# Performance work log

Measured on AMD Instinct MI355X. Metric: run time of the kernel, lower is better.

Reference implementation:

```python
import jax, jax.numpy as jnp
import numpy as np

N_NODES = 50000
N_EDGES = 640000
D_IN = 128
D_OUT = 128


def setup_inputs() -> dict:
    key = jax.random.key(0)
    k1, k2, k3, k4, k5, k6 = jax.random.split(key, 6)
    nfeat = jax.random.normal(k1, (N_NODES, D_IN), dtype=jnp.float32)
    w = jax.random.uniform(k2, (N_EDGES,), dtype=jnp.float32)
    # nn.Linear weights are [out_feats, in_feats], Kaiming-uniform-ish scale
    bound = 1.0 / np.sqrt(D_IN)
    W1 = jax.random.uniform(k3, (D_OUT, D_IN), dtype=jnp.float32, minval=-bound, maxval=bound)
    W2 = jax.random.uniform(k4, (D_OUT, D_IN), dtype=jnp.float32, minval=-bound, maxval=bound)
    src = jax.random.randint(k5, (N_EDGES,), 0, N_NODES, dtype=jnp.int64)
    dst = jax.random.randint(k6, (N_EDGES,), 0, N_NODES, dtype=jnp.int64)
    return {"nfeat": nfeat, "w": w, "W1": W1, "W2": W2, "src": src, "dst": dst}


def reference(nfeat, w, W1, W2, src, dst):
    # feat_drop is identity in eval mode
    h = nfeat  # [N, D_IN]
    # update_all(u_mul_e('h','w','m'), sum('m','h_neighbor')):
    # gather source features, scale by per-edge scalar weight, scatter-sum to dst
    msg = h[src] * w[:, None]                                   # [E, D_IN]
    h_neighbor = jax.ops.segment_sum(msg, dst, num_segments=h.shape[0])  # [N, D_IN]
    # Bi-interaction residual: leaky_relu(Linear(h + hn)) + leaky_relu(Linear(h * hn))
    add_branch = jax.nn.leaky_relu((h + h_neighbor) @ W1.T, negative_slope=0.01)
    mul_branch = jax.nn.leaky_relu((h * h_neighbor) @ W2.T, negative_slope=0.01)
    out = add_branch + mul_branch                                # [N, D_OUT]
    return (h_neighbor, out)
```

## Files before the change

kernel.cpp:

```cpp
#include <hip/hip_runtime.h>
#include <hip/hip_bf16.h>

#define N_NODES 50000
#define N_EDGES 640000
#define D 128
#define OUT0_ELEMS (N_NODES * D)
#define SCAN_BLOCKS ((N_NODES + 255) / 256)

typedef __attribute__((ext_vector_type(8))) short short8v;
typedef __attribute__((ext_vector_type(4))) short short4v;
typedef __attribute__((ext_vector_type(4))) float f32x4;

static __device__ __forceinline__ unsigned short f2bf(float x) {
  __hip_bfloat16 b = __float2bfloat16(x);
  return *reinterpret_cast<unsigned short*>(&b);
}
static __device__ __forceinline__ float bf2f(unsigned short u) {
  unsigned x = ((unsigned)u) << 16;
  return __builtin_bit_cast(float, x);
}
static __device__ __forceinline__ unsigned pack_edge(int s, float wv) {
  return ((unsigned)f2bf(wv) << 16) | (unsigned)s;
}

__global__ __launch_bounds__(256) void conv_all(
    const float* __restrict__ nfeat, const float* __restrict__ W1,
    const float* __restrict__ W2, unsigned short* __restrict__ nf16,
    unsigned short* __restrict__ wc, int* __restrict__ cnt) {
  int i = blockIdx.x * 256 + threadIdx.x;
  int base = i * 8;
  float4 a = *(const float4*)(nfeat + base);
  float4 b = *(const float4*)(nfeat + base + 4);
  short8v o;
  o[0] = (short)f2bf(a.x); o[1] = (short)f2bf(a.y);
  o[2] = (short)f2bf(a.z); o[3] = (short)f2bf(a.w);
  o[4] = (short)f2bf(b.x); o[5] = (short)f2bf(b.y);
  o[6] = (short)f2bf(b.z); o[7] = (short)f2bf(b.w);
  *(short8v*)(nf16 + base) = o;
  if (i < D * D) {
    wc[i] = f2bf(W1[i]);
    wc[D * D + i] = f2bf(W2[i]);
  }
  if (i < N_NODES) cnt[i] = 0;
}

__global__ __launch_bounds__(256) void hist_rank(
    const int* __restrict__ dst, int* __restrict__ cnt, int* __restrict__ rank) {
  int t = blockIdx.x * 256 + threadIdx.x;
  int e = t * 4;
  if (e >= N_EDGES) return;
  int4 d4 = *(const int4*)(dst + e);
  int4 r4;
  r4.x = atomicAdd(&cnt[d4.x], 1);
  r4.y = atomicAdd(&cnt[d4.y], 1);
  r4.z = atomicAdd(&cnt[d4.z], 1);
  r4.w = atomicAdd(&cnt[d4.w], 1);
  *(int4*)(rank + e) = r4;
}

__global__ __launch_bounds__(256) void scan_block(
    const int* __restrict__ cnt, int* __restrict__ offs, int* __restrict__ bsums) {
  __shared__ int sdata[256];
  int t = threadIdx.x;
  int i = blockIdx.x * 256 + t;
  int v = (i < N_NODES) ? cnt[i] : 0;
  sdata[t] = v;
  __syncthreads();
#pragma unroll
  for (int off = 1; off < 256; off <<= 1) {
    int x = (t >= off) ? sdata[t - off] : 0;
    __syncthreads();
    sdata[t] += x;
    __syncthreads();
  }
  if (i < N_NODES) offs[i] = sdata[t] - v;
  if (t == 255) bsums[blockIdx.x] = sdata[t];
}

__global__ __launch_bounds__(256) void scan_top(int* __restrict__ bsums) {
  __shared__ int sdata[256];
  int t = threadIdx.x;
  int v = (t < SCAN_BLOCKS) ? bsums[t] : 0;
  sdata[t] = v;
  __syncthreads();
#pragma unroll
  for (int off = 1; off < 256; off <<= 1) {
    int x = (t >= off) ? sdata[t - off] : 0;
    __syncthreads();
    sdata[t] += x;
    __syncthreads();
  }
  if (t < SCAN_BLOCKS) bsums[t] = sdata[t] - v;
}

__global__ __launch_bounds__(256) void scan_finalize(
    int* __restrict__ offs, const int* __restrict__ bsums) {
  int i = blockIdx.x * 256 + threadIdx.x;
  if (i >= N_NODES) return;
  offs[i] += bsums[blockIdx.x];
  if (i == N_NODES - 1) offs[N_NODES] = N_EDGES;
}

__global__ __launch_bounds__(256) void fill4(
    const int* __restrict__ src, const int* __restrict__ dst,
    const float* __restrict__ w, const int* __restrict__ rank,
    const int* __restrict__ offs, unsigned* __restrict__ es) {
  int t = blockIdx.x * 256 + threadIdx.x;
  int e = t * 4;
  if (e >= N_EDGES) return;
  int4 d4 = *(const int4*)(dst + e);
  int4 r4 = *(const int4*)(rank + e);
  int4 s4 = *(const int4*)(src + e);
  float4 w4 = *(const float4*)(w + e);
  es[offs[d4.x] + r4.x] = pack_edge(s4.x, w4.x);
  es[offs[d4.y] + r4.y] = pack_edge(s4.y, w4.y);
  es[offs[d4.z] + r4.z] = pack_edge(s4.z, w4.z);
  es[offs[d4.w] + r4.w] = pack_edge(s4.w, w4.w);
}

__global__ __launch_bounds__(256) void gather_bf16(
    const unsigned short* __restrict__ nf16, const int* __restrict__ offs,
    const unsigned* __restrict__ es, float* __restrict__ hn) {
  int tid = blockIdx.x * 256 + threadIdx.x;
  int node = tid >> 4;
  if (node >= N_NODES) return;
  int q = tid & 15;
  int beg = offs[node];
  int end = offs[node + 1];
  float acc[8];
#pragma unroll
  for (int j = 0; j < 8; ++j) acc[j] = 0.f;

  int k = beg;
  for (; k + 3 < end; k += 4) {
    unsigned r0 = es[k], r1 = es[k + 1], r2 = es[k + 2], r3 = es[k + 3];
    short8v v0 = *(const short8v*)(nf16 + (size_t)(r0 & 0xFFFF) * D + q * 8);
    short8v v1 = *(const short8v*)(nf16 + (size_t)(r1 & 0xFFFF) * D + q * 8);
    short8v v2 = *(const short8v*)(nf16 + (size_t)(r2 & 0xFFFF) * D + q * 8);
    short8v v3 = *(const short8v*)(nf16 + (size_t)(r3 & 0xFFFF) * D + q * 8);
    float w0 = bf2f((unsigned short)(r0 >> 16));
    float w1 = bf2f((unsigned short)(r1 >> 16));
    float w2 = bf2f((unsigned short)(r2 >> 16));
    float w3 = bf2f((unsigned short)(r3 >> 16));
#pragma unroll
    for (int j = 0; j < 8; ++j) {
      acc[j] += bf2f((unsigned short)v0[j]) * w0;
      acc[j] += bf2f((unsigned short)v1[j]) * w1;
      acc[j] += bf2f((unsigned short)v2[j]) * w2;
      acc[j] += bf2f((unsigned short)v3[j]) * w3;
    }
  }
  for (; k < end; ++k) {
    unsigned r0 = es[k];
    short8v v0 = *(const short8v*)(nf16 + (size_t)(r0 & 0xFFFF) * D + q * 8);
    float w0 = bf2f((unsigned short)(r0 >> 16));
#pragma unroll
    for (int j = 0; j < 8; ++j) acc[j] += bf2f((unsigned short)v0[j]) * w0;
  }

  float* orow = hn + (size_t)node * D + q * 8;
  *(float4*)(orow) = make_float4(acc[0], acc[1], acc[2], acc[3]);
  *(float4*)(orow + 4) = make_float4(acc[4], acc[5], acc[6], acc[7]);
}

__global__ __launch_bounds__(256) void gather_f32(
    const float* __restrict__ nfeat, const int* __restrict__ offs,
    const unsigned* __restrict__ es, float* __restrict__ hn) {
  int tid = blockIdx.x * 256 + threadIdx.x;
  int node = tid >> 5;
  if (node >= N_NODES) return;
  int q = tid & 31;
  int beg = offs[node];
  int end = offs[node + 1];
  float4 acc = {0.f, 0.f, 0.f, 0.f};
  int k = beg;
  for (; k + 1 < end; k += 2) {
    unsigned r0 = es[k], r1 = es[k + 1];
    float w0 = bf2f((unsigned short)(r0 >> 16));
    float w1 = bf2f((unsigned short)(r1 >> 16));
    float4 v0 = ((const float4*)(nfeat + (size_t)(r0 & 0xFFFF) * D))[q];
    float4 v1 = ((const float4*)(nfeat + (size_t)(r1 & 0xFFFF) * D))[q];
    acc.x += v0.x * w0 + v1.x * w1;
    acc.y += v0.y * w0 + v1.y * w1;
    acc.z += v0.z * w0 + v1.z * w1;
    acc.w += v0.w * w0 + v1.w * w1;
  }
  if (k < end) {
    unsigned r0 = es[k];
    float w0 = bf2f((unsigned short)(r0 >> 16));
    float4 v0 = ((const float4*)(nfeat + (size_t)(r0 & 0xFFFF) * D))[q];
    acc.x += v0.x * w0;
    acc.y += v0.y * w0;
    acc.z += v0.z * w0;
    acc.w += v0.w * w0;
  }
  ((float4*)(hn + (size_t)node * D))[q] = acc;
}

__global__ __launch_bounds__(256) void wconv(
    const float* __restrict__ W1, const float* __restrict__ W2,
    unsigned short* __restrict__ wc, int* __restrict__ cnt) {
  int i = blockIdx.x * 256 + threadIdx.x;
  if (i < D * D) {
    wc[i] = f2bf(W1[i]);
    wc[D * D + i] = f2bf(W2[i]);
  }
  if (i < N_NODES) cnt[i] = 0;
}

template <bool HBF16>
__global__ __launch_bounds__(256) void bi_mfma(
    const void* __restrict__ hsrc, const float* __restrict__ hn,
    const unsigned short* __restrict__ wc, float* __restrict__ out) {
  __shared__ __align__(16) unsigned short lds[2 * 64 * D];

  const int tid = threadIdx.x;
  const int lane = tid & 63;
  const int wid = tid >> 6;
  const int base = blockIdx.x * 64;
  const int r16 = lane & 15;
  const int kg = lane >> 4;

  short8v bf[2][2][4];
  {
    const int colbase = wid * 32;
#pragma unroll
    for (int g = 0; g < 2; ++g)
#pragma unroll
      for (int c = 0; c < 2; ++c)
#pragma unroll
        for (int ks = 0; ks < 4; ++ks) {
          int col = colbase + c * 16 + r16;
          int k = ks * 32 + kg * 8;
          bf[g][c][ks] =
              *(const short8v*)(wc + (size_t)g * D * D + (size_t)col * D + k);
        }
  }

#pragma unroll
  for (int p = 0; p < 8; ++p) {
    int flat = p * 1024 + tid * 4;
    int row = flat >> 7;
    int col = flat & 127;
    int node = base + row;
    float hx0 = 0.f, hx1 = 0.f, hx2 = 0.f, hx3 = 0.f;
    float4 nv = make_float4(0.f, 0.f, 0.f, 0.f);
    if (node < N_NODES) {
      if constexpr (HBF16) {
        short4v hv =
            *(const short4v*)((const unsigned short*)hsrc + (size_t)node * D + col);
        hx0 = bf2f((unsigned short)hv[0]);
        hx1 = bf2f((unsigned short)hv[1]);
        hx2 = bf2f((unsigned short)hv[2]);
        hx3 = bf2f((unsigned short)hv[3]);
      } else {
        float4 hv = *(const float4*)((const float*)hsrc + (size_t)node * D + col);
        hx0 = hv.x; hx1 = hv.y; hx2 = hv.z; hx3 = hv.w;
      }
      nv = *(const float4*)(hn + (size_t)node * D + col);
    }
    short4v av, mv;
    av[0] = (short)f2bf(hx0 + nv.x);
    av[1] = (short)f2bf(hx1 + nv.y);
    av[2] = (short)f2bf(hx2 + nv.z);
    av[3] = (short)f2bf(hx3 + nv.w);
    mv[0] = (short)f2bf(hx0 * nv.x);
    mv[1] = (short)f2bf(hx1 * nv.y);
    mv[2] = (short)f2bf(hx2 * nv.z);
    mv[3] = (short)f2bf(hx3 * nv.w);
    int boff = (row * 256 + col * 2) ^ ((row & 7) << 4);
    *(short4v*)((char*)lds + boff) = av;
    *(short4v*)((char*)lds + 16384 + boff) = mv;
  }
  __syncthreads();

  f32x4 acc1[4][2], acc2[4][2];
#pragma unroll
  for (int rt = 0; rt < 4; ++rt)
#pragma unroll
    for (int c = 0; c < 2; ++c) {
      acc1[rt][c] = (f32x4){0.f, 0.f, 0.f, 0.f};
      acc2[rt][c] = (f32x4){0.f, 0.f, 0.f, 0.f};
    }

#pragma unroll
  for (int ks = 0; ks < 4; ++ks) {
#pragma unroll
    for (int rt = 0; rt < 4; ++rt) {
      int row = rt * 16 + r16;
      int boff = (row * 256 + (ks * 32 + kg * 8) * 2) ^ ((row & 7) << 4);
      short8v a1 = *(const short8v*)((const char*)lds + boff);
      short8v a2 = *(const short8v*)((const char*)lds + 16384 + boff);
#pragma unroll
      for (int c = 0; c < 2; ++c) {
        acc1[rt][c] = __builtin_amdgcn_mfma_f32_16x16x32_bf16(
            a1, bf[0][c][ks], acc1[rt][c], 0, 0, 0);
        acc2[rt][c] = __builtin_amdgcn_mfma_f32_16x16x32_bf16(
            a2, bf[1][c][ks], acc2[rt][c], 0, 0, 0);
      }
    }
  }

#pragma unroll
  for (int rt = 0; rt < 4; ++rt) {
#pragma unroll
    for (int c = 0; c < 2; ++c) {
#pragma unroll
      for (int e = 0; e < 4; ++e) {
        int row = rt * 16 + kg * 4 + e;
        int node = base + row;
        if (node < N_NODES) {
          int col = wid * 32 + c * 16 + r16;
          float x1 = acc1[rt][c][e];
          float x2 = acc2[rt][c][e];
          x1 = x1 > 0.f ? x1 : 0.01f * x1;
          x2 = x2 > 0.f ? x2 : 0.01f * x2;
          out[(size_t)node * D + col] = x1 + x2;
        }
      }
    }
  }
}

__global__ __launch_bounds__(256) void edge_scatter(
    const float* __restrict__ nfeat, const float* __restrict__ w,
    const int* __restrict__ src, const int* __restrict__ dst,
    float* __restrict__ hn) {
  int tid = blockIdx.x * 256 + threadIdx.x;
  int e = tid >> 5;
  if (e >= N_EDGES) return;
  int q = tid & 31;
  int s = src[e];
  int d = dst[e];
  float we = w[e];
  float4 v = ((const float4*)(nfeat + (size_t)s * D))[q];
  float* drow = hn + (size_t)d * D + q * 4;
  atomicAdd(drow + 0, v.x * we);
  atomicAdd(drow + 1, v.y * we);
  atomicAdd(drow + 2, v.z * we);
  atomicAdd(drow + 3, v.w * we);
}

__global__ __launch_bounds__(256) void bi_inter(
    const float* __restrict__ h, const float* __restrict__ hn,
    const float* __restrict__ W1, const float* __restrict__ W2,
    float* __restrict__ out) {
  int wid = __builtin_amdgcn_readfirstlane(threadIdx.x >> 6);
  int lane = threadIdx.x & 63;
  int node = blockIdx.x * 64 + lane;
  if (node >= N_NODES) return;
  const float4* h4 = (const float4*)(h + (size_t)node * D);
  const float4* n4 = (const float4*)(hn + (size_t)node * D);
  float acc1[32], acc2[32];
#pragma unroll
  for (int j = 0; j < 32; ++j) { acc1[j] = 0.f; acc2[j] = 0.f; }
  const int obase = wid * 32;
  for (int kq = 0; kq < 32; ++kq) {
    float4 hv = h4[kq];
    float4 nv = n4[kq];
    float a0 = hv.x + nv.x, a1 = hv.y + nv.y, a2 = hv.z + nv.z, a3 = hv.w + nv.w;
    float m0 = hv.x * nv.x, m1 = hv.y * nv.y, m2 = hv.z * nv.z, m3 = hv.w * nv.w;
#pragma unroll
    for (int j = 0; j < 32; ++j) {
      int o = obase + j;
      float4 w1 = *(const float4*)(W1 + (size_t)o * D + kq * 4);
      float4 w2 = *(const float4*)(W2 + (size_t)o * D + kq * 4);
      acc1[j] += a0 * w1.x + a1 * w1.y + a2 * w1.z + a3 * w1.w;
      acc2[j] += m0 * w2.x + m1 * w2.y + m2 * w2.z + m3 * w2.w;
    }
  }
  float* orow = out + (size_t)node * D + obase;
#pragma unroll
  for (int j = 0; j < 32; j += 4) {
    float4 r;
    float x;
    x = acc1[j + 0]; x = x > 0.f ? x : 0.01f * x;
    r.x = x; x = acc2[j + 0]; x = x > 0.f ? x : 0.01f * x; r.x += x;
    x = acc1[j + 1]; x = x > 0.f ? x : 0.01f * x;
    r.y = x; x = acc2[j + 1]; x = x > 0.f ? x : 0.01f * x; r.y += x;
    x = acc1[j + 2]; x = x > 0.f ? x : 0.01f * x;
    r.z = x; x = acc2[j + 2]; x = x > 0.f ? x : 0.01f * x; r.z += x;
    x = acc1[j + 3]; x = x > 0.f ? x : 0.01f * x;
    r.w = x; x = acc2[j + 3]; x = x > 0.f ? x : 0.01f * x; r.w += x;
    *(float4*)(orow + j) = r;
  }
}

extern "C" void kernel_launch(void* const* d_in, const int* in_sizes, int n_in,
                              void* d_out, int out_size, void* d_ws, size_t ws_size,
                              hipStream_t stream) {
  const float* nfeat = (const float*)d_in[0];
  const float* w     = (const float*)d_in[1];
  const float* W1    = (const float*)d_in[2];
  const float* W2    = (const float*)d_in[3];
  const int*   src   = (const int*)d_in[4];
  const int*   dst   = (const int*)d_in[5];

  float* hn  = (float*)d_out;
  float* out = (float*)d_out + OUT0_ELEMS;

  char* ws = (char*)d_ws;
  size_t off = 0;
  int* cnt = (int*)(ws + off);        off += (size_t)N_NODES * 4;
  int* offs = (int*)(ws + off);       off += (size_t)(N_NODES + 1) * 4;
  int* bsums = (int*)(ws + off);      off += 256 * 4;
  int* rank = (int*)(ws + off);       off += (size_t)N_EDGES * 4;
  unsigned* es = (unsigned*)(ws + off); off += (size_t)N_EDGES * 4;
  off = (off + 63) & ~(size_t)63;
  unsigned short* wc = (unsigned short*)(ws + off);
  off += (size_t)2 * D * D * 2;
  size_t tier1_bytes = off;
  off = (off + 63) & ~(size_t)63;
  unsigned short* nf16 = (unsigned short*)(ws + off);
  off += (size_t)N_NODES * D * 2;
  size_t tier2_bytes = off;

  if (ws_size < tier1_bytes) {
    hipMemsetAsync(hn, 0, (size_t)OUT0_ELEMS * sizeof(float), stream);
    long long threads = (long long)N_EDGES * 32;
    int blocks = (int)((threads + 255) / 256);
    edge_scatter<<<blocks, 256, 0, stream>>>(nfeat, w, src, dst, hn);
    bi_inter<<<(N_NODES + 63) / 64, 256, 0, stream>>>(nfeat, hn, W1, W2, out);
    return;
  }

  bool full = (ws_size >= tier2_bytes);

  if (full) {
    conv_all<<<N_NODES * D / 8 / 256, 256, 0, stream>>>(
        nfeat, W1, W2, nf16, wc, cnt);
  } else {
    wconv<<<(N_NODES + 255) / 256, 256, 0, stream>>>(W1, W2, wc, cnt);
  }
  hist_rank<<<N_EDGES / 4 / 256, 256, 0, stream>>>(dst, cnt, rank);
  scan_block<<<SCAN_BLOCKS, 256, 0, stream>>>(cnt, offs, bsums);
  scan_top<<<1, 256, 0, stream>>>(bsums);
  scan_finalize<<<SCAN_BLOCKS, 256, 0, stream>>>(offs, bsums);
  fill4<<<N_EDGES / 4 / 256, 256, 0, stream>>>(src, dst, w, rank, offs, es);

  if (full) {
    gather_bf16<<<(N_NODES * 16 + 255) / 256, 256, 0, stream>>>(nf16, offs, es, hn);
    bi_mfma<true><<<(N_NODES + 63) / 64, 256, 0, stream>>>(nf16, hn, wc, out);
  } else {
    gather_f32<<<(N_NODES * 32 + 255) / 256, 256, 0, stream>>>(nfeat, offs, es, hn);
    bi_mfma<false><<<(N_NODES + 63) / 64, 256, 0, stream>>>(nfeat, hn, wc, out);
  }
}
```

Baseline: 111.1 us.

## Fuse neighbor gather into bi-interaction MFMA kernel and collapse scan into one kernel

Merges the bf16 gather kernel with the bi-interaction MFMA kernel. Each block aggregates neighbor features for its 64 nodes, writes hn, and places h+hn and h*hn straight into LDS as bf16, so the MFMA stage no longer reads hn back from global memory. The three-kernel prefix scan is replaced by a single 256-thread block in which each thread serially scans a chunk of 196 counts. The cost is fewer, heavier gather blocks with lower parallelism (one node per 16 threads across 4 iterations), and a scan that runs serially on one block.

```diff
diff --git a/kernel.cpp b/kernel.cpp
--- a/kernel.cpp
+++ b/kernel.cpp
@@ -5,7 +5,7 @@
 #define N_EDGES 640000
 #define D 128
 #define OUT0_ELEMS (N_NODES * D)
-#define SCAN_BLOCKS ((N_NODES + 255) / 256)
+#define SCAN_CHUNK 196
 
 typedef __attribute__((ext_vector_type(8))) short short8v;
 typedef __attribute__((ext_vector_type(4))) short short4v;
@@ -58,13 +58,16 @@
   *(int4*)(rank + e) = r4;
 }
 
-__global__ __launch_bounds__(256) void scan_block(
-    const int* __restrict__ cnt, int* __restrict__ offs, int* __restrict__ bsums) {
+__global__ __launch_bounds__(256) void scan_one(
+    const int* __restrict__ cnt, int* __restrict__ offs) {
   __shared__ int sdata[256];
   int t = threadIdx.x;
-  int i = blockIdx.x * 256 + t;
-  int v = (i < N_NODES) ? cnt[i] : 0;
-  sdata[t] = v;
+  int beg = t * SCAN_CHUNK;
+  int end = beg + SCAN_CHUNK;
+  if (end > N_NODES) end = N_NODES;
+  int s = 0;
+  for (int i = beg; i < end; ++i) s += cnt[i];
+  sdata[t] = s;
   __syncthreads();
 #pragma unroll
   for (int off = 1; off < 256; off <<= 1) {
@@ -73,32 +76,12 @@
     sdata[t] += x;
     __syncthreads();
   }
-  if (i < N_NODES) offs[i] = sdata[t] - v;
-  if (t == 255) bsums[blockIdx.x] = sdata[t];
-}
-
-__global__ __launch_bounds__(256) void scan_top(int* __restrict__ bsums) {
-  __shared__ int sdata[256];
-  int t = threadIdx.x;
-  int v = (t < SCAN_BLOCKS) ? bsums[t] : 0;
-  sdata[t] = v;
-  __syncthreads();
-#pragma unroll
-  for (int off = 1; off < 256; off <<= 1) {
-    int x = (t >= off) ? sdata[t - off] : 0;
-    __syncthreads();
-    sdata[t] += x;
-    __syncthreads();
-  }
-  if (t < SCAN_BLOCKS) bsums[t] = sdata[t] - v;
-}
-
-__global__ __launch_bounds__(256) void scan_finalize(
-    int* __restrict__ offs, const int* __restrict__ bsums) {
-  int i = blockIdx.x * 256 + threadIdx.x;
-  if (i >= N_NODES) return;
-  offs[i] += bsums[blockIdx.x];
-  if (i == N_NODES - 1) offs[N_NODES] = N_EDGES;
+  int run = sdata[t] - s;
+  for (int i = beg; i < end; ++i) {
+    offs[i] = run;
+    run += cnt[i];
+  }
+  if (t == 0) offs[N_NODES] = N_EDGES;
 }
 
 __global__ __launch_bounds__(256) void fill4(
@@ -118,49 +101,156 @@
   es[offs[d4.w] + r4.w] = pack_edge(s4.w, w4.w);
 }
 
-__global__ __launch_bounds__(256) void gather_bf16(
+__global__ __launch_bounds__(256) void gather_bi(
     const unsigned short* __restrict__ nf16, const int* __restrict__ offs,
-    const unsigned* __restrict__ es, float* __restrict__ hn) {
-  int tid = blockIdx.x * 256 + threadIdx.x;
-  int node = tid >> 4;
-  if (node >= N_NODES) return;
-  int q = tid & 15;
-  int beg = offs[node];
-  int end = offs[node + 1];
-  float acc[8];
-#pragma unroll
-  for (int j = 0; j < 8; ++j) acc[j] = 0.f;
-
-  int k = beg;
-  for (; k + 3 < end; k += 4) {
-    unsigned r0 = es[k], r1 = es[k + 1], r2 = es[k + 2], r3 = es[k + 3];
-    short8v v0 = *(const short8v*)(nf16 + (size_t)(r0 & 0xFFFF) * D + q * 8);
-    short8v v1 = *(const short8v*)(nf16 + (size_t)(r1 & 0xFFFF) * D + q * 8);
-    short8v v2 = *(const short8v*)(nf16 + (size_t)(r2 & 0xFFFF) * D + q * 8);
-    short8v v3 = *(const short8v*)(nf16 + (size_t)(r3 & 0xFFFF) * D + q * 8);
-    float w0 = bf2f((unsigned short)(r0 >> 16));
-    float w1 = bf2f((unsigned short)(r1 >> 16));
-    float w2 = bf2f((unsigned short)(r2 >> 16));
-    float w3 = bf2f((unsigned short)(r3 >> 16));
+    const unsigned* __restrict__ es, const unsigned short* __restrict__ wc,
+    float* __restrict__ hn, float* __restrict__ out) {
+  __shared__ __align__(16) unsigned short lds[2 * 64 * D];
+
+  const int tid = threadIdx.x;
+  const int base = blockIdx.x * 64;
+  const int g = tid >> 4;
+  const int q = tid & 15;
+
+#pragma unroll
+  for (int i = 0; i < 4; ++i) {
+    int row = g * 4 + i;
+    int node = base + row;
+    float acc[8];
+#pragma unroll
+    for (int j = 0; j < 8; ++j) acc[j] = 0.f;
+    float hx[8];
+#pragma unroll
+    for (int j = 0; j < 8; ++j) hx[j] = 0.f;
+
+    if (node < N_NODES) {
+      int beg = offs[node];
+      int end = offs[node + 1];
+      int k = beg;
+      for (; k + 3 < end; k += 4) {
+        unsigned r0 = es[k], r1 = es[k + 1], r2 = es[k + 2], r3 = es[k + 3];
+        short8v v0 = *(const short8v*)(nf16 + (size_t)(r0 & 0xFFFF) * D + q * 8);
+        short8v v1 = *(const short8v*)(nf16 + (size_t)(r1 & 0xFFFF) * D + q * 8);
+        short8v v2 = *(const short8v*)(nf16 + (size_t)(r2 & 0xFFFF) * D + q * 8);
+        short8v v3 = *(const short8v*)(nf16 + (size_t)(r3 & 0xFFFF) * D + q * 8);
+        float w0 = bf2f((unsigned short)(r0 >> 16));
+        float w1 = bf2f((unsigned short)(r1 >> 16));
+        float w2 = bf2f((unsigned short)(r2 >> 16));
+        float w3 = bf2f((unsigned short)(r3 >> 16));
+#pragma unroll
+        for (int j = 0; j < 8; ++j) {
+          acc[j] += bf2f((unsigned short)v0[j]) * w0;
+          acc[j] += bf2f((unsigned short)v1[j]) * w1;
+          acc[j] += bf2f((unsigned short)v2[j]) * w2;
+          acc[j] += bf2f((unsigned short)v3[j]) * w3;
+        }
+      }
+      for (; k < end; ++k) {
+        unsigned r0 = es[k];
+        short8v v0 = *(const short8v*)(nf16 + (size_t)(r0 & 0xFFFF) * D + q * 8);
+        float w0 = bf2f((unsigned short)(r0 >> 16));
+#pragma unroll
+        for (int j = 0; j < 8; ++j) acc[j] += bf2f((unsigned short)v0[j]) * w0;
+      }
+
+      short8v hv = *(const short8v*)(nf16 + (size_t)node * D + q * 8);
+#pragma unroll
+      for (int j = 0; j < 8; ++j) hx[j] = bf2f((unsigned short)hv[j]);
+
+      float* orow = hn + (size_t)node * D + q * 8;
+      *(float4*)(orow) = make_float4(acc[0], acc[1], acc[2], acc[3]);
+      *(float4*)(orow + 4) = make_float4(acc[4], acc[5], acc[6], acc[7]);
+    }
+
+    short8v av, mv;
 #pragma unroll
     for (int j = 0; j < 8; ++j) {
-      acc[j] += bf2f((unsigned short)v0[j]) * w0;
-      acc[j] += bf2f((unsigned short)v1[j]) * w1;
-      acc[j] += bf2f((unsigned short)v2[j]) * w2;
-      acc[j] += bf2f((unsigned short)v3[j]) * w3;
-    }
-  }
-  for (; k < end; ++k) {
-    unsigned r0 = es[k];
-    short8v v0 = *(const short8v*)(nf16 + (size_t)(r0 & 0xFFFF) * D + q * 8);
-    float w0 = bf2f((unsigned short)(r0 >> 16));
-#pragma unroll
-    for (int j = 0; j < 8; ++j) acc[j] += bf2f((unsigned short)v0[j]) * w0;
-  }
-
-  float* orow = hn + (size_t)node * D + q * 8;
-  *(float4*)(orow) = make_float4(acc[0], acc[1], acc[2], acc[3]);
-  *(float4*)(orow + 4) = make_float4(acc[4], acc[5], acc[6], acc[7]);
+      av[j] = (short)f2bf(hx[j] + acc[j]);
+      mv[j] = (short)f2bf(hx[j] * acc[j]);
+    }
+    int boff = (row * 256 + q * 16) ^ ((row & 7) << 4);
+    *(short8v*)((char*)lds + boff) = av;
+    *(short8v*)((char*)lds + 16384 + boff) = mv;
+  }
+
+  const int lane = tid & 63;
+  const int wid = tid >> 6;
+  const int r16 = lane & 15;
+  const int kg = lane >> 4;
+  short8v bf[2][2][4];
+  {
+    const int colbase = wid * 32;
+#pragma unroll
+    for (int gg = 0; gg < 2; ++gg)
+#pragma unroll
+      for (int c = 0; c < 2; ++c)
+#pragma unroll
+        for (int ks = 0; ks < 4; ++ks) {
+          int col = colbase + c * 16 + r16;
+          int k = ks * 32 + kg * 8;
+          bf[gg][c][ks] =
+              *(const short8v*)(wc + (size_t)gg * D * D + (size_t)col * D + k);
+        }
+  }
+  __syncthreads();
+
+  f32x4 acc1[4][2], acc2[4][2];
+#pragma unroll
+  for (int rt = 0; rt < 4; ++rt)
+#pragma unroll
+    for (int c = 0; c < 2; ++c) {
+      acc1[rt][c] = (f32x4){0.f, 0.f, 0.f, 0.f};
+      acc2[rt][c] = (f32x4){0.f, 0.f, 0.f, 0.f};
+    }
+
+#pragma unroll
+  for (int ks = 0; ks < 4; ++ks) {
+#pragma unroll
+    for (int rt = 0; rt < 4; ++rt) {
+      int row = rt * 16 + r16;
+      int boff = (row * 256 + (ks * 32 + kg * 8) * 2) ^ ((row & 7) << 4);
+      short8v a1 = *(const short8v*)((const char*)lds + boff);
+      short8v a2 = *(const short8v*)((const char*)lds + 16384 + boff);
+#pragma unroll
+      for (int c = 0; c < 2; ++c) {
+        acc1[rt][c] = __builtin_amdgcn_mfma_f32_16x16x32_bf16(
+            a1, bf[0][c][ks], acc1[rt][c], 0, 0, 0);
+        acc2[rt][c] = __builtin_amdgcn_mfma_f32_16x16x32_bf16(
+            a2, bf[1][c][ks], acc2[rt][c], 0, 0, 0);
+      }
+    }
+  }
+
+#pragma unroll
+  for (int rt = 0; rt < 4; ++rt) {
+#pragma unroll
+    for (int c = 0; c < 2; ++c) {
+#pragma unroll
+      for (int e = 0; e < 4; ++e) {
+        int row = rt * 16 + kg * 4 + e;
+        int node = base + row;
+        if (node < N_NODES) {
+          int col = wid * 32 + c * 16 + r16;
+          float x1 = acc1[rt][c][e];
+          float x2 = acc2[rt][c][e];
+          x1 = x1 > 0.f ? x1 : 0.01f * x1;
+          x2 = x2 > 0.f ? x2 : 0.01f * x2;
+          out[(size_t)node * D + col] = x1 + x2;
+        }
+      }
+    }
+  }
+}
+
+__global__ __launch_bounds__(256) void wconv(
+    const float* __restrict__ W1, const float* __restrict__ W2,
+    unsigned short* __restrict__ wc, int* __restrict__ cnt) {
+  int i = blockIdx.x * 256 + threadIdx.x;
+  if (i < D * D) {
+    wc[i] = f2bf(W1[i]);
+    wc[D * D + i] = f2bf(W2[i]);
+  }
+  if (i < N_NODES) cnt[i] = 0;
 }
 
 __global__ __launch_bounds__(256) void gather_f32(
@@ -197,46 +287,31 @@
   ((float4*)(hn + (size_t)node * D))[q] = acc;
 }
 
-__global__ __launch_bounds__(256) void wconv(
-    const float* __restrict__ W1, const float* __restrict__ W2,
-    unsigned short* __restrict__ wc, int* __restrict__ cnt) {
-  int i = blockIdx.x * 256 + threadIdx.x;
-  if (i < D * D) {
-    wc[i] = f2bf(W1[i]);
-    wc[D * D + i] = f2bf(W2[i]);
-  }
-  if (i < N_NODES) cnt[i] = 0;
-}
-
-template <bool HBF16>
-__global__ __launch_bounds__(256) void bi_mfma(
-    const void* __restrict__ hsrc, const float* __restrict__ hn,
+__global__ __launch_bounds__(256) void bi_mfma_f32(
+    const float* __restrict__ h, const float* __restrict__ hn,
     const unsigned short* __restrict__ wc, float* __restrict__ out) {
   __shared__ __align__(16) unsigned short lds[2 * 64 * D];
-
   const int tid = threadIdx.x;
   const int lane = tid & 63;
   const int wid = tid >> 6;
   const int base = blockIdx.x * 64;
   const int r16 = lane & 15;
   const int kg = lane >> 4;
-
   short8v bf[2][2][4];
   {
     const int colbase = wid * 32;
 #pragma unroll
-    for (int g = 0; g < 2; ++g)
+    for (int gg = 0; gg < 2; ++gg)
 #pragma unroll
       for (int c = 0; c < 2; ++c)
 #pragma unroll
         for (int ks = 0; ks < 4; ++ks) {
           int col = colbase + c * 16 + r16;
           int k = ks * 32 + kg * 8;
-          bf[g][c][ks] =
-              *(const short8v*)(wc + (size_t)g * D * D + (size_t)col * D + k);
+          bf[gg][c][ks] =
+              *(const short8v*)(wc + (size_t)gg * D * D + (size_t)col * D + k);
         }
   }
-
 #pragma unroll
   for (int p = 0; p < 8; ++p) {
     int flat = p * 1024 + tid * 4;
@@ -246,17 +321,8 @@
     float hx0 = 0.f, hx1 = 0.f, hx2 = 0.f, hx3 = 0.f;
     float4 nv = make_float4(0.f, 0.f, 0.f, 0.f);
     if (node < N_NODES) {
-      if constexpr (HBF16) {
-        short4v hv =
-            *(const short4v*)((const unsigned short*)hsrc + (size_t)node * D + col);
-        hx0 = bf2f((unsigned short)hv[0]);
-        hx1 = bf2f((unsigned short)hv[1]);
-        hx2 = bf2f((unsigned short)hv[2]);
-        hx3 = bf2f((unsigned short)hv[3]);
-      } else {
-        float4 hv = *(const float4*)((const float*)hsrc + (size_t)node * D + col);
-        hx0 = hv.x; hx1 = hv.y; hx2 = hv.z; hx3 = hv.w;
-      }
+      float4 hv = *(const float4*)(h + (size_t)node * D + col);
+      hx0 = hv.x; hx1 = hv.y; hx2 = hv.z; hx3 = hv.w;
       nv = *(const float4*)(hn + (size_t)node * D + col);
     }
     short4v av, mv;
@@ -273,7 +339,6 @@
     *(short4v*)((char*)lds + 16384 + boff) = mv;
   }
   __syncthreads();
-
   f32x4 acc1[4][2], acc2[4][2];
 #pragma unroll
   for (int rt = 0; rt < 4; ++rt)
@@ -282,7 +347,6 @@
       acc1[rt][c] = (f32x4){0.f, 0.f, 0.f, 0.f};
       acc2[rt][c] = (f32x4){0.f, 0.f, 0.f, 0.f};
     }
-
 #pragma unroll
   for (int ks = 0; ks < 4; ++ks) {
 #pragma unroll
@@ -300,7 +364,6 @@
       }
     }
   }
-
 #pragma unroll
   for (int rt = 0; rt < 4; ++rt) {
 #pragma unroll
@@ -401,10 +464,9 @@
 
   char* ws = (char*)d_ws;
   size_t off = 0;
-  int* cnt = (int*)(ws + off);        off += (size_t)N_NODES * 4;
-  int* offs = (int*)(ws + off);       off += (size_t)(N_NODES + 1) * 4;
-  int* bsums = (int*)(ws + off);      off += 256 * 4;
-  int* rank = (int*)(ws + off);       off += (size_t)N_EDGES * 4;
+  int* cnt = (int*)(ws + off);          off += (size_t)N_NODES * 4;
+  int* offs = (int*)(ws + off);         off += (size_t)(N_NODES + 1) * 4;
+  int* rank = (int*)(ws + off);         off += (size_t)N_EDGES * 4;
   unsigned* es = (unsigned*)(ws + off); off += (size_t)N_EDGES * 4;
   off = (off + 63) & ~(size_t)63;
   unsigned short* wc = (unsigned short*)(ws + off);
@@ -433,16 +495,13 @@
     wconv<<<(N_NODES + 255) / 256, 256, 0, stream>>>(W1, W2, wc, cnt);
   }
   hist_rank<<<N_EDGES / 4 / 256, 256, 0, stream>>>(dst, cnt, rank);
-  scan_block<<<SCAN_BLOCKS, 256, 0, stream>>>(cnt, offs, bsums);
-  scan_top<<<1, 256, 0, stream>>>(bsums);
-  scan_finalize<<<SCAN_BLOCKS, 256, 0, stream>>>(offs, bsums);
+  scan_one<<<1, 256, 0, stream>>>(cnt, offs);
   fill4<<<N_EDGES / 4 / 256, 256, 0, stream>>>(src, dst, w, rank, offs, es);
 
   if (full) {
-    gather_bf16<<<(N_NODES * 16 + 255) / 256, 256, 0, stream>>>(nf16, offs, es, hn);
-    bi_mfma<true><<<(N_NODES + 63) / 64, 256, 0, stream>>>(nf16, hn, wc, out);
+    gather_bi<<<(N_NODES + 63) / 64, 256, 0, stream>>>(nf16, offs, es, wc, hn, out);
   } else {
     gather_f32<<<(N_NODES * 32 + 255) / 256, 256, 0, stream>>>(nfeat, offs, es, hn);
-    bi_mfma<false><<<(N_NODES + 63) / 64, 256, 0, stream>>>(nfeat, hn, wc, out);
-  }
-}
+    bi_mfma_f32<<<(N_NODES + 63) / 64, 256, 0, stream>>>(nfeat, hn, wc, out);
+  }
+}
```

New measurement: 196.7 us. +77.1%, slower.

## Fuse CSR build stages into one persistent kernel with software grid barriers

Applied to the files above, without the earlier changes.

Merges the bf16 conversion, histogram/rank, two-level scan and edge fill kernels into a single persistent kernel of 512 blocks that separates phases with atomic-based grid barriers. The scan is restructured into per-block chunk sums, a single-block top scan, and a local rescan. The goal is to remove several kernel launches and the gaps between them. In exchange it relies on all 512 blocks being co-resident and adds barrier spin costs; the intermediate fp32 fallback tier is dropped.

```diff
diff --git a/kernel.cpp b/kernel.cpp
--- a/kernel.cpp
+++ b/kernel.cpp
@@ -5,7 +5,10 @@
 #define N_EDGES 640000
 #define D 128
 #define OUT0_ELEMS (N_NODES * D)
-#define SCAN_BLOCKS ((N_NODES + 255) / 256)
+
+#define CSR_BLOCKS 512
+#define CSR_THREADS (CSR_BLOCKS * 256)
+#define CHUNK 98
 
 typedef __attribute__((ext_vector_type(8))) short short8v;
 typedef __attribute__((ext_vector_type(4))) short short4v;
@@ -23,99 +26,128 @@
   return ((unsigned)f2bf(wv) << 16) | (unsigned)s;
 }
 
-__global__ __launch_bounds__(256) void conv_all(
+static __device__ __forceinline__ void grid_sync(int* bar, int phase) {
+  __syncthreads();
+  if (threadIdx.x == 0) {
+    int prev = __hip_atomic_fetch_add(&bar[0], 1, __ATOMIC_ACQ_REL,
+                                      __HIP_MEMORY_SCOPE_AGENT);
+    if (prev == (int)gridDim.x - 1) {
+      __hip_atomic_store(&bar[0], 0, __ATOMIC_RELAXED, __HIP_MEMORY_SCOPE_AGENT);
+      __hip_atomic_store(&bar[1], phase, __ATOMIC_RELEASE, __HIP_MEMORY_SCOPE_AGENT);
+    } else {
+      long long guard = 0;
+      while (__hip_atomic_load(&bar[1], __ATOMIC_ACQUIRE,
+                               __HIP_MEMORY_SCOPE_AGENT) < phase) {
+        __builtin_amdgcn_s_sleep(4);
+        if (++guard > (1LL << 28)) break;
+      }
+    }
+  }
+  __syncthreads();
+}
+
+__global__ __launch_bounds__(256, 2) void build_all(
     const float* __restrict__ nfeat, const float* __restrict__ W1,
-    const float* __restrict__ W2, unsigned short* __restrict__ nf16,
-    unsigned short* __restrict__ wc, int* __restrict__ cnt) {
-  int i = blockIdx.x * 256 + threadIdx.x;
-  int base = i * 8;
-  float4 a = *(const float4*)(nfeat + base);
-  float4 b = *(const float4*)(nfeat + base + 4);
-  short8v o;
-  o[0] = (short)f2bf(a.x); o[1] = (short)f2bf(a.y);
-  o[2] = (short)f2bf(a.z); o[3] = (short)f2bf(a.w);
-  o[4] = (short)f2bf(b.x); o[5] = (short)f2bf(b.y);
-  o[6] = (short)f2bf(b.z); o[7] = (short)f2bf(b.w);
-  *(short8v*)(nf16 + base) = o;
-  if (i < D * D) {
-    wc[i] = f2bf(W1[i]);
-    wc[D * D + i] = f2bf(W2[i]);
-  }
-  if (i < N_NODES) cnt[i] = 0;
-}
-
-__global__ __launch_bounds__(256) void hist_rank(
-    const int* __restrict__ dst, int* __restrict__ cnt, int* __restrict__ rank) {
-  int t = blockIdx.x * 256 + threadIdx.x;
-  int e = t * 4;
-  if (e >= N_EDGES) return;
-  int4 d4 = *(const int4*)(dst + e);
-  int4 r4;
-  r4.x = atomicAdd(&cnt[d4.x], 1);
-  r4.y = atomicAdd(&cnt[d4.y], 1);
-  r4.z = atomicAdd(&cnt[d4.z], 1);
-  r4.w = atomicAdd(&cnt[d4.w], 1);
-  *(int4*)(rank + e) = r4;
-}
-
-__global__ __launch_bounds__(256) void scan_block(
-    const int* __restrict__ cnt, int* __restrict__ offs, int* __restrict__ bsums) {
+    const float* __restrict__ W2, const int* __restrict__ src,
+    const int* __restrict__ dst, const float* __restrict__ w,
+    unsigned short* __restrict__ nf16, unsigned short* __restrict__ wc,
+    int* __restrict__ cnt, int* __restrict__ offs, int* __restrict__ rank,
+    unsigned* __restrict__ es, int* __restrict__ bsums, int* __restrict__ bar) {
+  const int tid = threadIdx.x;
+  const int t = blockIdx.x * 256 + tid;
   __shared__ int sdata[256];
-  int t = threadIdx.x;
-  int i = blockIdx.x * 256 + t;
-  int v = (i < N_NODES) ? cnt[i] : 0;
-  sdata[t] = v;
-  __syncthreads();
-#pragma unroll
-  for (int off = 1; off < 256; off <<= 1) {
-    int x = (t >= off) ? sdata[t - off] : 0;
+
+  if (t < N_NODES) cnt[t] = 0;
+  if (t < D * D) {
+    wc[t] = f2bf(W1[t]);
+    wc[D * D + t] = f2bf(W2[t]);
+  }
+  for (int u = t; u < N_NODES * D / 8; u += CSR_THREADS) {
+    int base = u * 8;
+    float4 a = *(const float4*)(nfeat + base);
+    float4 b = *(const float4*)(nfeat + base + 4);
+    short8v o;
+    o[0] = (short)f2bf(a.x); o[1] = (short)f2bf(a.y);
+    o[2] = (short)f2bf(a.z); o[3] = (short)f2bf(a.w);
+    o[4] = (short)f2bf(b.x); o[5] = (short)f2bf(b.y);
+    o[6] = (short)f2bf(b.z); o[7] = (short)f2bf(b.w);
+    *(short8v*)(nf16 + base) = o;
+  }
+  grid_sync(bar, 1);
+
+  for (int u = t; u < N_EDGES / 4; u += CSR_THREADS) {
+    int e = u * 4;
+    int4 d4 = *(const int4*)(dst + e);
+    int4 r4;
+    r4.x = atomicAdd(&cnt[d4.x], 1);
+    r4.y = atomicAdd(&cnt[d4.y], 1);
+    r4.z = atomicAdd(&cnt[d4.z], 1);
+    r4.w = atomicAdd(&cnt[d4.w], 1);
+    *(int4*)(rank + e) = r4;
+  }
+  grid_sync(bar, 2);
+
+  {
+    int i = blockIdx.x * CHUNK + tid;
+    int v = (tid < CHUNK && i < N_NODES) ? cnt[i] : 0;
+    sdata[tid] = v;
     __syncthreads();
-    sdata[t] += x;
+#pragma unroll
+    for (int o = 128; o > 0; o >>= 1) {
+      if (tid < o) sdata[tid] += sdata[tid + o];
+      __syncthreads();
+    }
+    if (tid == 0) bsums[blockIdx.x] = sdata[0];
+  }
+  grid_sync(bar, 3);
+
+  if (blockIdx.x == 0) {
+    int b0 = bsums[2 * tid], b1 = bsums[2 * tid + 1];
+    int p = b0 + b1;
+    sdata[tid] = p;
     __syncthreads();
-  }
-  if (i < N_NODES) offs[i] = sdata[t] - v;
-  if (t == 255) bsums[blockIdx.x] = sdata[t];
-}
-
-__global__ __launch_bounds__(256) void scan_top(int* __restrict__ bsums) {
-  __shared__ int sdata[256];
-  int t = threadIdx.x;
-  int v = (t < SCAN_BLOCKS) ? bsums[t] : 0;
-  sdata[t] = v;
-  __syncthreads();
-#pragma unroll
-  for (int off = 1; off < 256; off <<= 1) {
-    int x = (t >= off) ? sdata[t - off] : 0;
+#pragma unroll
+    for (int o = 1; o < 256; o <<= 1) {
+      int x = (tid >= o) ? sdata[tid - o] : 0;
+      __syncthreads();
+      sdata[tid] += x;
+      __syncthreads();
+    }
+    int excl = sdata[tid] - p;
+    bsums[2 * tid] = excl;
+    bsums[2 * tid + 1] = excl + b0;
+  }
+  grid_sync(bar, 4);
+
+  {
+    int i = blockIdx.x * CHUNK + tid;
+    int v = (tid < CHUNK && i < N_NODES) ? cnt[i] : 0;
+    sdata[tid] = v;
     __syncthreads();
-    sdata[t] += x;
-    __syncthreads();
-  }
-  if (t < SCAN_BLOCKS) bsums[t] = sdata[t] - v;
-}
-
-__global__ __launch_bounds__(256) void scan_finalize(
-    int* __restrict__ offs, const int* __restrict__ bsums) {
-  int i = blockIdx.x * 256 + threadIdx.x;
-  if (i >= N_NODES) return;
-  offs[i] += bsums[blockIdx.x];
-  if (i == N_NODES - 1) offs[N_NODES] = N_EDGES;
-}
-
-__global__ __launch_bounds__(256) void fill4(
-    const int* __restrict__ src, const int* __restrict__ dst,
-    const float* __restrict__ w, const int* __restrict__ rank,
-    const int* __restrict__ offs, unsigned* __restrict__ es) {
-  int t = blockIdx.x * 256 + threadIdx.x;
-  int e = t * 4;
-  if (e >= N_EDGES) return;
-  int4 d4 = *(const int4*)(dst + e);
-  int4 r4 = *(const int4*)(rank + e);
-  int4 s4 = *(const int4*)(src + e);
-  float4 w4 = *(const float4*)(w + e);
-  es[offs[d4.x] + r4.x] = pack_edge(s4.x, w4.x);
-  es[offs[d4.y] + r4.y] = pack_edge(s4.y, w4.y);
-  es[offs[d4.z] + r4.z] = pack_edge(s4.z, w4.z);
-  es[offs[d4.w] + r4.w] = pack_edge(s4.w, w4.w);
+#pragma unroll
+    for (int o = 1; o < 256; o <<= 1) {
+      int x = (tid >= o) ? sdata[tid - o] : 0;
+      __syncthreads();
+      sdata[tid] += x;
+      __syncthreads();
+    }
+    int excl = sdata[tid] - v + bsums[blockIdx.x];
+    if (tid < CHUNK && i < N_NODES) offs[i] = excl;
+    if (t == 0) offs[N_NODES] = N_EDGES;
+  }
+  grid_sync(bar, 5);
+
+  for (int u = t; u < N_EDGES / 4; u += CSR_THREADS) {
+    int e = u * 4;
+    int4 d4 = *(const int4*)(dst + e);
+    int4 r4 = *(const int4*)(rank + e);
+    int4 s4 = *(const int4*)(src + e);
+    float4 w4 = *(const float4*)(w + e);
+    es[offs[d4.x] + r4.x] = pack_edge(s4.x, w4.x);
+    es[offs[d4.y] + r4.y] = pack_edge(s4.y, w4.y);
+    es[offs[d4.z] + r4.z] = pack_edge(s4.z, w4.z);
+    es[offs[d4.w] + r4.w] = pack_edge(s4.w, w4.w);
+  }
 }
 
 __global__ __launch_bounds__(256) void gather_bf16(
@@ -163,54 +195,8 @@
   *(float4*)(orow + 4) = make_float4(acc[4], acc[5], acc[6], acc[7]);
 }
 
-__global__ __launch_bounds__(256) void gather_f32(
-    const float* __restrict__ nfeat, const int* __restrict__ offs,
-    const unsigned* __restrict__ es, float* __restrict__ hn) {
-  int tid = blockIdx.x * 256 + threadIdx.x;
-  int node = tid >> 5;
-  if (node >= N_NODES) return;
-  int q = tid & 31;
-  int beg = offs[node];
-  int end = offs[node + 1];
-  float4 acc = {0.f, 0.f, 0.f, 0.f};
-  int k = beg;
-  for (; k + 1 < end; k += 2) {
-    unsigned r0 = es[k], r1 = es[k + 1];
-    float w0 = bf2f((unsigned short)(r0 >> 16));
-    float w1 = bf2f((unsigned short)(r1 >> 16));
-    float4 v0 = ((const float4*)(nfeat + (size_t)(r0 & 0xFFFF) * D))[q];
-    float4 v1 = ((const float4*)(nfeat + (size_t)(r1 & 0xFFFF) * D))[q];
-    acc.x += v0.x * w0 + v1.x * w1;
-    acc.y += v0.y * w0 + v1.y * w1;
-    acc.z += v0.z * w0 + v1.z * w1;
-    acc.w += v0.w * w0 + v1.w * w1;
-  }
-  if (k < end) {
-    unsigned r0 = es[k];
-    float w0 = bf2f((unsigned short)(r0 >> 16));
-    float4 v0 = ((const float4*)(nfeat + (size_t)(r0 & 0xFFFF) * D))[q];
-    acc.x += v0.x * w0;
-    acc.y += v0.y * w0;
-    acc.z += v0.z * w0;
-    acc.w += v0.w * w0;
-  }
-  ((float4*)(hn + (size_t)node * D))[q] = acc;
-}
-
-__global__ __launch_bounds__(256) void wconv(
-    const float* __restrict__ W1, const float* __restrict__ W2,
-    unsigned short* __restrict__ wc, int* __restrict__ cnt) {
-  int i = blockIdx.x * 256 + threadIdx.x;
-  if (i < D * D) {
-    wc[i] = f2bf(W1[i]);
-    wc[D * D + i] = f2bf(W2[i]);
-  }
-  if (i < N_NODES) cnt[i] = 0;
-}
-
-template <bool HBF16>
-__global__ __launch_bounds__(256) void bi_mfma(
-    const void* __restrict__ hsrc, const float* __restrict__ hn,
+__global__ __launch_bounds__(256) void bi_mfma_h16(
+    const unsigned short* __restrict__ h16, const float* __restrict__ hn,
     const unsigned short* __restrict__ wc, float* __restrict__ out) {
   __shared__ __align__(16) unsigned short lds[2 * 64 * D];
 
@@ -246,17 +232,11 @@
     float hx0 = 0.f, hx1 = 0.f, hx2 = 0.f, hx3 = 0.f;
     float4 nv = make_float4(0.f, 0.f, 0.f, 0.f);
     if (node < N_NODES) {
-      if constexpr (HBF16) {
-        short4v hv =
-            *(const short4v*)((const unsigned short*)hsrc + (size_t)node * D + col);
-        hx0 = bf2f((unsigned short)hv[0]);
-        hx1 = bf2f((unsigned short)hv[1]);
-        hx2 = bf2f((unsigned short)hv[2]);
-        hx3 = bf2f((unsigned short)hv[3]);
-      } else {
-        float4 hv = *(const float4*)((const float*)hsrc + (size_t)node * D + col);
-        hx0 = hv.x; hx1 = hv.y; hx2 = hv.z; hx3 = hv.w;
-      }
+      short4v hv = *(const short4v*)(h16 + (size_t)node * D + col);
+      hx0 = bf2f((unsigned short)hv[0]);
+      hx1 = bf2f((unsigned short)hv[1]);
+      hx2 = bf2f((unsigned short)hv[2]);
+      hx3 = bf2f((unsigned short)hv[3]);
       nv = *(const float4*)(hn + (size_t)node * D + col);
     }
     short4v av, mv;
@@ -401,21 +381,21 @@
 
   char* ws = (char*)d_ws;
   size_t off = 0;
-  int* cnt = (int*)(ws + off);        off += (size_t)N_NODES * 4;
-  int* offs = (int*)(ws + off);       off += (size_t)(N_NODES + 1) * 4;
-  int* bsums = (int*)(ws + off);      off += 256 * 4;
-  int* rank = (int*)(ws + off);       off += (size_t)N_EDGES * 4;
+  int* bar = (int*)(ws + off);          off += 64;
+  int* bsums = (int*)(ws + off);        off += CSR_BLOCKS * 4;
+  int* cnt = (int*)(ws + off);          off += (size_t)N_NODES * 4;
+  int* offs = (int*)(ws + off);         off += (size_t)(N_NODES + 1) * 4;
+  int* rank = (int*)(ws + off);         off += (size_t)N_EDGES * 4;
   unsigned* es = (unsigned*)(ws + off); off += (size_t)N_EDGES * 4;
   off = (off + 63) & ~(size_t)63;
   unsigned short* wc = (unsigned short*)(ws + off);
   off += (size_t)2 * D * D * 2;
-  size_t tier1_bytes = off;
   off = (off + 63) & ~(size_t)63;
   unsigned short* nf16 = (unsigned short*)(ws + off);
   off += (size_t)N_NODES * D * 2;
-  size_t tier2_bytes = off;
-
-  if (ws_size < tier1_bytes) {
+  size_t full_bytes = off;
+
+  if (ws_size < full_bytes) {
     hipMemsetAsync(hn, 0, (size_t)OUT0_ELEMS * sizeof(float), stream);
     long long threads = (long long)N_EDGES * 32;
     int blocks = (int)((threads + 255) / 256);
@@ -424,25 +404,10 @@
     return;
   }
 
-  bool full = (ws_size >= tier2_bytes);
-
-  if (full) {
-    conv_all<<<N_NODES * D / 8 / 256, 256, 0, stream>>>(
-        nfeat, W1, W2, nf16, wc, cnt);
-  } else {
-    wconv<<<(N_NODES + 255) / 256, 256, 0, stream>>>(W1, W2, wc, cnt);
-  }
-  hist_rank<<<N_EDGES / 4 / 256, 256, 0, stream>>>(dst, cnt, rank);
-  scan_block<<<SCAN_BLOCKS, 256, 0, stream>>>(cnt, offs, bsums);
-  scan_top<<<1, 256, 0, stream>>>(bsums);
-  scan_finalize<<<SCAN_BLOCKS, 256, 0, stream>>>(offs, bsums);
-  fill4<<<N_EDGES / 4 / 256, 256, 0, stream>>>(src, dst, w, rank, offs, es);
-
-  if (full) {
-    gather_bf16<<<(N_NODES * 16 + 255) / 256, 256, 0, stream>>>(nf16, offs, es, hn);
-    bi_mfma<true><<<(N_NODES + 63) / 64, 256, 0, stream>>>(nf16, hn, wc, out);
-  } else {
-    gather_f32<<<(N_NODES * 32 + 255) / 256, 256, 0, stream>>>(nfeat, offs, es, hn);
-    bi_mfma<false><<<(N_NODES + 63) / 64, 256, 0, stream>>>(nfeat, hn, wc, out);
-  }
-}
+  hipMemsetAsync(bar, 0, 16, stream);
+
+  build_all<<<CSR_BLOCKS, 256, 0, stream>>>(
+      nfeat, W1, W2, src, dst, w, nf16, wc, cnt, offs, rank, es, bsums, bar);
+  gather_bf16<<<(N_NODES * 16 + 255) / 256, 256, 0, stream>>>(nf16, offs, es, hn);
+  bi_mfma_h16<<<(N_NODES + 63) / 64, 256, 0, stream>>>(nf16, hn, wc, out);
+}
```

Result: slower. 324.0 us (+191.6%).
